# Performance work log

Measured on AMD Instinct MI355X. Metric: run time of the kernel, lower is better.

The kernel has to match this reference:

```python
import jax, jax.numpy as jnp
import numpy as np

LATENT, D_MODEL, WIN, ENC_IN, BATCH = 128, 512, 256, 55, 256


def setup_inputs() -> dict:
    key = jax.random.key(0)
    ks = jax.random.split(key, 9)
    sl = lambda k, shape, fan_in: (jax.random.normal(k, shape, jnp.float32) / np.sqrt(fan_in)).astype(jnp.float32)
    return {
        "z": jax.random.normal(ks[0], (BATCH, LATENT), jnp.float32),
        "h_proj_w": sl(ks[1], (D_MODEL, LATENT), LATENT),
        "h_proj_b": sl(ks[2], (D_MODEL,), LATENT),
        "w_ih": sl(ks[3], (3 * D_MODEL, D_MODEL), D_MODEL),
        "w_hh": sl(ks[4], (3 * D_MODEL, D_MODEL), D_MODEL),
        "b_ih": sl(ks[5], (3 * D_MODEL,), D_MODEL),
        "b_hh": sl(ks[6], (3 * D_MODEL,), D_MODEL),
        "out_w": sl(ks[7], (ENC_IN, D_MODEL), D_MODEL),
        "out_b": sl(ks[8], (ENC_IN,), D_MODEL),
        "win_size": WIN,
    }


def reference(z, h_proj_w, h_proj_b, w_ih, w_hh, b_ih, b_hh, out_w, out_b, win_size):
    d = h_proj_w.shape[0]
    # h0 = tanh(Linear(z)) -> [B, d]
    h0 = jnp.tanh(z @ h_proj_w.T + h_proj_b)
    # GRU input is all zeros, so input-gate preactivation is just b_ih
    # (w_ih @ 0 == 0); gate order in torch GRU is (r, z, n).
    gi_r, gi_z, gi_n = b_ih[:d], b_ih[d:2 * d], b_ih[2 * d:]

    def step(h, _):
        gh = h @ w_hh.T + b_hh                      # [B, 3d]
        r = jax.nn.sigmoid(gi_r + gh[:, :d])
        zg = jax.nn.sigmoid(gi_z + gh[:, d:2 * d])
        n = jnp.tanh(gi_n + r * gh[:, 2 * d:])
        h_new = (1.0 - zg) * n + zg * h
        return h_new, h_new

    _, hs = jax.lax.scan(step, h0, None, length=win_size)  # [T, B, d]
    hs = jnp.transpose(hs, (1, 0, 2))                      # [B, T, d]
    return hs @ out_w.T + out_b                            # [B, T, enc_in]
```

## Files before the change

### kernel.cpp

```cpp
#include <hip/hip_runtime.h>

#define DM     512
#define LAT    128
#define WIN_   256
#define ENC    55
#define GB     32
#define BT     8
#define DS     64
#define TPB    768
#define OUT_T  256
#define AROW16 528
#define GHS    200
#define OWS    520
#define NK     22
#define NKP    24

typedef __attribute__((ext_vector_type(8))) short bf8;
typedef __attribute__((ext_vector_type(4))) float f4;
typedef unsigned long long u64;
typedef unsigned short u16;

__device__ __align__(128) u64 g_ring2[2][GB][8][BT][NKP];
__device__ __align__(128) u64 g_lcnt[GB * 8 * 16];

__device__ __forceinline__ u16 f2bf(float f) {
    union { float f; unsigned int i; } v; v.f = f;
    unsigned int r = v.i + 0x7fffu + ((v.i >> 16) & 1u);
    return (u16)(r >> 16);
}
__device__ __forceinline__ float sigm(float x) { return 1.f / (1.f + __expf(-x)); }
__device__ __forceinline__ float tanh_(float x) {
    x = fminf(x, 40.f);
    float e = __expf(2.f * x);
    return (e - 1.f) / (e + 1.f);
}
#define ALOAD(p)     __hip_atomic_load((p),      __ATOMIC_RELAXED, __HIP_MEMORY_SCOPE_AGENT)
#define ASTORE(p, v) __hip_atomic_store((p), (v), __ATOMIC_RELAXED, __HIP_MEMORY_SCOPE_AGENT)

__global__ __launch_bounds__(TPB, 3) void gru_fused(
    const float* __restrict__ z,
    const float* __restrict__ hpw,
    const float* __restrict__ hpb,
    const float* __restrict__ whh,
    const float* __restrict__ bih,
    const float* __restrict__ bhh,
    const float* __restrict__ outw,
    const float* __restrict__ outb,
    float* __restrict__ out)
{
    const int blk  = blockIdx.x;
    const int g    = blk & (GB - 1);
    const int s    = blk >> 5;
    const int d0   = s * DS;
    const int row0 = g * BT;
    const int tid  = threadIdx.x;
    const int wave = tid >> 6;
    const int lane = tid & 63;
    const int quad = lane >> 4;
    const int nl   = lane & 15;

    __shared__ __align__(16) u16 sm16[BT * AROW16];
    __shared__ __align__(16) float ghT[BT][GHS];
    __shared__ float bias_r[DS], bias_z[DS], gin_[DS], bhn_[DS];
    __shared__ __align__(16) u16 hpack[BT][66];
    __shared__ __align__(16) u16 sOutW[ENC * OWS];
    __shared__ float sOutB[64];
    __shared__ u64 sh_lc;

    u64* lc_own = g_lcnt + (u64)(g * 8 + s) * 16;
    if (tid == 0) sh_lc = ALOAD(lc_own);

    if (tid < DS) {
        int dg = d0 + tid;
        bias_r[tid] = bih[dg]       + bhh[dg];
        bias_z[tid] = bih[512 + dg] + bhh[512 + dg];
        gin_[tid]   = bih[1024 + dg];
        bhn_[tid]   = bhh[1024 + dg];
    }
    if (tid < ENC) sOutB[tid] = outb[tid];
    for (int i = tid; i < ENC * DM; i += TPB)
        sOutW[(i >> 9) * OWS + (i & 511)] = f2bf(outw[i]);

    const int gl   = wave * 16 + nl;
    const int sel  = gl >> 6;
    const int jrow = sel * 512 + d0 + (gl & 63);
    bf8 bfrag[16];
#pragma unroll
    for (int kb = 0; kb < 16; ++kb) {
        const float* wp = whh + jrow * DM + kb * 32 + quad * 8;
        bf8 v;
#pragma unroll
        for (int j = 0; j < 8; ++j) v[j] = (short)f2bf(wp[j]);
        bfrag[kb] = v;
    }
    __syncthreads();

    const u64 base = sh_lc * 512ULL + 1ULL;
    float hprev_reg = 0.f;

    if (wave < BT) {
        float acc = hpb[d0 + lane];
        const float* zr = z + (row0 + wave) * LAT;
        const float* wr = hpw + (d0 + lane) * LAT;
#pragma unroll 8
        for (int k = 0; k < LAT; ++k) acc += zr[k] * wr[k];
        hprev_reg = tanh_(acc);
        if (lane < 2) hpack[wave][64 + lane] = 0;
        hpack[wave][lane] = f2bf(hprev_reg);
        const u16 sq = (u16)base;
        if (lane < NK) {
            u16 b0 = hpack[wave][3 * lane], b1 = hpack[wave][3 * lane + 1],
                b2 = hpack[wave][3 * lane + 2];
            u64 rec = (u64)sq | ((u64)b0 << 16) | ((u64)b1 << 32) | ((u64)b2 << 48);
            ASTORE(&g_ring2[0][g][s][wave][lane], rec);
        }
    }

    const u16* afrag_base = sm16 + (nl & 7) * AROW16;

    for (int t = 1; t <= WIN_; ++t) {
        const int sp = (t - 1) & 1, sc = t & 1;
        const u16 want = (u16)(base + t - 1);

        if (wave < BT)
            sm16[wave * AROW16 + d0 + lane] = f2bf(hprev_reg);
        if (wave >= 1 && wave < 8) {
            const int j = (s + wave) & 7;
            const u64* rb = &g_ring2[sp][g][j][0][0];
            const int row = lane >> 3, k = lane & 7;
            {
                const u64* pp = rb + 7 * NKP + 21;
                long guard = 0;
                while ((u16)ALOAD(pp) != want && guard < (1L << 18)) ++guard;
            }
            const u64* p0 = rb + row * NKP + k;
            const bool v2 = (k + 16) < NK;
            u64 r0 = ALOAD(p0), r1 = ALOAD(p0 + 8), r2 = v2 ? ALOAD(p0 + 16) : 0;
            bool ok0 = ((u16)r0 == want), ok1 = ((u16)r1 == want),
                 ok2 = (!v2) || ((u16)r2 == want);
            long guard = 0;
            while (!__all(ok0 && ok1 && ok2) && guard < (1L << 18)) {
                if (!ok0) { r0 = ALOAD(p0);      ok0 = ((u16)r0 == want); }
                if (!ok1) { r1 = ALOAD(p0 + 8);  ok1 = ((u16)r1 == want); }
                if (!ok2) { r2 = ALOAD(p0 + 16); ok2 = ((u16)r2 == want); }
                ++guard;
            }
            u16* dst = sm16 + row * AROW16 + j * 64;
            int db = 3 * k;
            dst[db] = (u16)(r0 >> 16); dst[db + 1] = (u16)(r0 >> 32); dst[db + 2] = (u16)(r0 >> 48);
            db = 3 * (k + 8);
            dst[db] = (u16)(r1 >> 16); dst[db + 1] = (u16)(r1 >> 32); dst[db + 2] = (u16)(r1 >> 48);
            if (v2) {
                db = 3 * (k + 16);
                dst[db] = (u16)(r2 >> 16);
                if (db + 1 < DS) dst[db + 1] = (u16)(r2 >> 32);
                if (db + 2 < DS) dst[db + 2] = (u16)(r2 >> 48);
            }
        }
        __syncthreads();

        f4 acc = {0.f, 0.f, 0.f, 0.f};
#pragma unroll
        for (int kb = 0; kb < 16; ++kb) {
            bf8 av = *(const bf8*)(afrag_base + quad * 8 + kb * 32);
            acc = __builtin_amdgcn_mfma_f32_16x16x32_bf16(av, bfrag[kb], acc, 0, 0, 0);
        }
        if (quad < 2) {
#pragma unroll
            for (int r = 0; r < 4; ++r) ghT[quad * 4 + r][gl] = acc[r];
        }
        __syncthreads();

        if (wave < BT) {
            const int d = lane;
            const float* grow = &ghT[wave][0];
            float rr = sigm(bias_r[d] + grow[d]);
            float zg = sigm(bias_z[d] + grow[64 + d]);
            float nn = tanh_(gin_[d] + rr * (bhn_[d] + grow[128 + d]));
            float h  = (1.f - zg) * nn + zg * hprev_reg;
            hprev_reg = h;
            hpack[wave][d] = f2bf(h);
            const u16 sq = (u16)(base + t);
            if (lane < NK) {
                u16 b0 = hpack[wave][3 * lane], b1 = hpack[wave][3 * lane + 1],
                    b2 = hpack[wave][3 * lane + 2];
                u64 rec = (u64)sq | ((u64)b0 << 16) | ((u64)b1 << 32) | ((u64)b2 << 48);
                ASTORE(&g_ring2[sc][g][s][wave][lane], rec);
            }
        }

        const int tau = t - 2;
        const bool proj = (tau >= 0) && ((tau & 7) == s);
        if (proj && wave >= 8) {
            const int e  = (wave - 8) * 16 + nl;
            const int ec = (e < ENC) ? e : (ENC - 1);
            const u16* wrow = sOutW + ec * OWS + quad * 8;
            f4 accp = {0.f, 0.f, 0.f, 0.f};
#pragma unroll
            for (int kb = 0; kb < 16; ++kb) {
                bf8 av = *(const bf8*)(afrag_base + quad * 8 + kb * 32);
                bf8 wv = *(const bf8*)(wrow + kb * 32);
                accp = __builtin_amdgcn_mfma_f32_16x16x32_bf16(av, wv, accp, 0, 0, 0);
            }
            if (quad < 2 && e < ENC) {
                float ob = sOutB[e];
#pragma unroll
                for (int r = 0; r < 4; ++r) {
                    int m = quad * 4 + r;
                    out[(row0 + m) * (OUT_T * ENC) + tau * ENC + e] = accp[r] + ob;
                }
            }
        }
        if (proj) __syncthreads();
    }

    if (s == 7) {
        const u16 want = (u16)(base + WIN_);
        if (wave < BT)
            sm16[wave * AROW16 + d0 + lane] = f2bf(hprev_reg);
        if (wave >= 1 && wave < 8) {
            const int j = (s + wave) & 7;
            const u64* rb = &g_ring2[0][g][j][0][0];
            const int row = lane >> 3, k = lane & 7;
            {
                const u64* pp = rb + 7 * NKP + 21;
                long guard = 0;
                while ((u16)ALOAD(pp) != want && guard < (1L << 18)) ++guard;
            }
            const u64* p0 = rb + row * NKP + k;
            const bool v2 = (k + 16) < NK;
            u64 r0 = ALOAD(p0), r1 = ALOAD(p0 + 8), r2 = v2 ? ALOAD(p0 + 16) : 0;
            bool ok0 = ((u16)r0 == want), ok1 = ((u16)r1 == want),
                 ok2 = (!v2) || ((u16)r2 == want);
            long guard = 0;
            while (!__all(ok0 && ok1 && ok2) && guard < (1L << 18)) {
                if (!ok0) { r0 = ALOAD(p0);      ok0 = ((u16)r0 == want); }
                if (!ok1) { r1 = ALOAD(p0 + 8);  ok1 = ((u16)r1 == want); }
                if (!ok2) { r2 = ALOAD(p0 + 16); ok2 = ((u16)r2 == want); }
                ++guard;
            }
            u16* dst = sm16 + row * AROW16 + j * 64;
            int db = 3 * k;
            dst[db] = (u16)(r0 >> 16); dst[db + 1] = (u16)(r0 >> 32); dst[db + 2] = (u16)(r0 >> 48);
            db = 3 * (k + 8);
            dst[db] = (u16)(r1 >> 16); dst[db + 1] = (u16)(r1 >> 32); dst[db + 2] = (u16)(r1 >> 48);
            if (v2) {
                db = 3 * (k + 16);
                dst[db] = (u16)(r2 >> 16);
                if (db + 1 < DS) dst[db + 1] = (u16)(r2 >> 32);
                if (db + 2 < DS) dst[db + 2] = (u16)(r2 >> 48);
            }
        }
        __syncthreads();
        if (wave >= 8) {
            const int e  = (wave - 8) * 16 + nl;
            const int ec = (e < ENC) ? e : (ENC - 1);
            const u16* wrow = sOutW + ec * OWS + quad * 8;
            f4 accp = {0.f, 0.f, 0.f, 0.f};
#pragma unroll
            for (int kb = 0; kb < 16; ++kb) {
                bf8 av = *(const bf8*)(afrag_base + quad * 8 + kb * 32);
                bf8 wv = *(const bf8*)(wrow + kb * 32);
                accp = __builtin_amdgcn_mfma_f32_16x16x32_bf16(av, wv, accp, 0, 0, 0);
            }
            if (quad < 2 && e < ENC) {
                float ob = sOutB[e];
#pragma unroll
                for (int r = 0; r < 4; ++r) {
                    int m = quad * 4 + r;
                    out[(row0 + m) * (OUT_T * ENC) + 255 * ENC + e] = accp[r] + ob;
                }
            }
        }
    }

    if (tid == 0) ASTORE(lc_own, sh_lc + 1ULL);
}

extern "C" void kernel_launch(void* const* d_in, const int* in_sizes, int n_in,
                              void* d_out, int out_size, void* d_ws, size_t ws_size,
                              hipStream_t stream) {
    const float* z    = (const float*)d_in[0];
    const float* hpw  = (const float*)d_in[1];
    const float* hpb  = (const float*)d_in[2];
    const float* whh  = (const float*)d_in[4];
    const float* bih  = (const float*)d_in[5];
    const float* bhh  = (const float*)d_in[6];
    const float* outw = (const float*)d_in[7];
    const float* outb = (const float*)d_in[8];
    float* out = (float*)d_out;

    (void)d_ws; (void)ws_size;
    gru_fused<<<dim3(256), dim3(TPB), 0, stream>>>(
        z, hpw, hpb, whh, bih, bhh, outw, outb, out);
}
```

Measured before the change: 705.0 us.

## Streamline per-step sync: lighter barriers, shuffle packing, speculative ring loads

Replaces __syncthreads with a barrier that waits only on LDS counters, so outstanding global stores do not stall the workgroup barrier. Packs the bf16 hidden-state records with wave shuffles instead of an LDS staging buffer. Polls the ring by loading the sentinel and the payload together, cutting a round trip of global latency per step. Splits the MFMA chain into two accumulators to expose more instruction-level parallelism. It adds an explicit vmcnt wait before publishing and relies on memory-ordering assumptions that could be fragile.

```diff
diff --git a/kernel.cpp b/kernel.cpp
--- a/kernel.cpp
+++ b/kernel.cpp
@@ -36,6 +36,50 @@
 }
 #define ALOAD(p)     __hip_atomic_load((p),      __ATOMIC_RELAXED, __HIP_MEMORY_SCOPE_AGENT)
 #define ASTORE(p, v) __hip_atomic_store((p), (v), __ATOMIC_RELAXED, __HIP_MEMORY_SCOPE_AGENT)
+
+__device__ __forceinline__ void bar_lgkm() {
+    __builtin_amdgcn_sched_barrier(0);
+    asm volatile("s_waitcnt lgkmcnt(0)" ::: "memory");
+    __builtin_amdgcn_s_barrier();
+    __builtin_amdgcn_sched_barrier(0);
+}
+
+__device__ __forceinline__ void fetch_slice(const u64* rb, u16 want, u16* sm,
+                                            int j, int lane) {
+    const int row = lane >> 3, k = lane & 7;
+    const u64* pp = rb + 7 * NKP + 21;
+    const u64* p0 = rb + row * NKP + k;
+    const bool v2 = (k + 16) < NK;
+    u64 r0 = 0, r1 = 0, r2 = 0;
+    long guard = 0;
+    for (;;) {
+        u64 bc = ALOAD(pp);
+        r0 = ALOAD(p0);
+        r1 = ALOAD(p0 + 8);
+        r2 = v2 ? ALOAD(p0 + 16) : 0;
+        if ((u16)bc == want || ++guard >= (1L << 18)) break;
+    }
+    bool ok0 = ((u16)r0 == want), ok1 = ((u16)r1 == want),
+         ok2 = (!v2) || ((u16)r2 == want);
+    guard = 0;
+    while (!__all(ok0 && ok1 && ok2) && guard < (1L << 18)) {
+        if (!ok0) { r0 = ALOAD(p0);      ok0 = ((u16)r0 == want); }
+        if (!ok1) { r1 = ALOAD(p0 + 8);  ok1 = ((u16)r1 == want); }
+        if (!ok2) { r2 = ALOAD(p0 + 16); ok2 = ((u16)r2 == want); }
+        ++guard;
+    }
+    u16* dst = sm + row * AROW16 + j * 64;
+    int db = 3 * k;
+    dst[db] = (u16)(r0 >> 16); dst[db + 1] = (u16)(r0 >> 32); dst[db + 2] = (u16)(r0 >> 48);
+    db = 3 * (k + 8);
+    dst[db] = (u16)(r1 >> 16); dst[db + 1] = (u16)(r1 >> 32); dst[db + 2] = (u16)(r1 >> 48);
+    if (v2) {
+        db = 3 * (k + 16);
+        dst[db] = (u16)(r2 >> 16);
+        if (db + 1 < DS) dst[db + 1] = (u16)(r2 >> 32);
+        if (db + 2 < DS) dst[db + 2] = (u16)(r2 >> 48);
+    }
+}
 
 __global__ __launch_bounds__(TPB, 3) void gru_fused(
     const float* __restrict__ z,
@@ -62,7 +106,6 @@
     __shared__ __align__(16) u16 sm16[BT * AROW16];
     __shared__ __align__(16) float ghT[BT][GHS];
     __shared__ float bias_r[DS], bias_z[DS], gin_[DS], bhn_[DS];
-    __shared__ __align__(16) u16 hpack[BT][66];
     __shared__ __align__(16) u16 sOutW[ENC * OWS];
     __shared__ float sOutB[64];
     __shared__ u64 sh_lc;
@@ -93,7 +136,7 @@
         for (int j = 0; j < 8; ++j) v[j] = (short)f2bf(wp[j]);
         bfrag[kb] = v;
     }
-    __syncthreads();
+    bar_lgkm();
 
     const u64 base = sh_lc * 512ULL + 1ULL;
     float hprev_reg = 0.f;
@@ -105,13 +148,13 @@
 #pragma unroll 8
         for (int k = 0; k < LAT; ++k) acc += zr[k] * wr[k];
         hprev_reg = tanh_(acc);
-        if (lane < 2) hpack[wave][64 + lane] = 0;
-        hpack[wave][lane] = f2bf(hprev_reg);
-        const u16 sq = (u16)base;
+        int hbf = (int)f2bf(hprev_reg);
+        int b0 = __shfl(hbf, 3 * lane);
+        int b1 = __shfl(hbf, 3 * lane + 1);
+        int b2 = __shfl(hbf, 3 * lane + 2);
         if (lane < NK) {
-            u16 b0 = hpack[wave][3 * lane], b1 = hpack[wave][3 * lane + 1],
-                b2 = hpack[wave][3 * lane + 2];
-            u64 rec = (u64)sq | ((u64)b0 << 16) | ((u64)b1 << 32) | ((u64)b2 << 48);
+            u64 rec = (u64)(u16)base | ((u64)(u16)b0 << 16)
+                    | ((u64)(u16)b1 << 32) | ((u64)(u16)b2 << 48);
             ASTORE(&g_ring2[0][g][s][wave][lane], rec);
         }
     }
@@ -126,50 +169,24 @@
             sm16[wave * AROW16 + d0 + lane] = f2bf(hprev_reg);
         if (wave >= 1 && wave < 8) {
             const int j = (s + wave) & 7;
-            const u64* rb = &g_ring2[sp][g][j][0][0];
-            const int row = lane >> 3, k = lane & 7;
-            {
-                const u64* pp = rb + 7 * NKP + 21;
-                long guard = 0;
-                while ((u16)ALOAD(pp) != want && guard < (1L << 18)) ++guard;
-            }
-            const u64* p0 = rb + row * NKP + k;
-            const bool v2 = (k + 16) < NK;
-            u64 r0 = ALOAD(p0), r1 = ALOAD(p0 + 8), r2 = v2 ? ALOAD(p0 + 16) : 0;
-            bool ok0 = ((u16)r0 == want), ok1 = ((u16)r1 == want),
-                 ok2 = (!v2) || ((u16)r2 == want);
-            long guard = 0;
-            while (!__all(ok0 && ok1 && ok2) && guard < (1L << 18)) {
-                if (!ok0) { r0 = ALOAD(p0);      ok0 = ((u16)r0 == want); }
-                if (!ok1) { r1 = ALOAD(p0 + 8);  ok1 = ((u16)r1 == want); }
-                if (!ok2) { r2 = ALOAD(p0 + 16); ok2 = ((u16)r2 == want); }
-                ++guard;
-            }
-            u16* dst = sm16 + row * AROW16 + j * 64;
-            int db = 3 * k;
-            dst[db] = (u16)(r0 >> 16); dst[db + 1] = (u16)(r0 >> 32); dst[db + 2] = (u16)(r0 >> 48);
-            db = 3 * (k + 8);
-            dst[db] = (u16)(r1 >> 16); dst[db + 1] = (u16)(r1 >> 32); dst[db + 2] = (u16)(r1 >> 48);
-            if (v2) {
-                db = 3 * (k + 16);
-                dst[db] = (u16)(r2 >> 16);
-                if (db + 1 < DS) dst[db + 1] = (u16)(r2 >> 32);
-                if (db + 2 < DS) dst[db + 2] = (u16)(r2 >> 48);
-            }
-        }
-        __syncthreads();
-
-        f4 acc = {0.f, 0.f, 0.f, 0.f};
-#pragma unroll
-        for (int kb = 0; kb < 16; ++kb) {
-            bf8 av = *(const bf8*)(afrag_base + quad * 8 + kb * 32);
-            acc = __builtin_amdgcn_mfma_f32_16x16x32_bf16(av, bfrag[kb], acc, 0, 0, 0);
+            fetch_slice(&g_ring2[sp][g][j][0][0], want, sm16, j, lane);
+        }
+        bar_lgkm();
+
+        f4 acc0 = {0.f, 0.f, 0.f, 0.f}, acc1 = {0.f, 0.f, 0.f, 0.f};
+#pragma unroll
+        for (int kb = 0; kb < 16; kb += 2) {
+            bf8 av0 = *(const bf8*)(afrag_base + quad * 8 + kb * 32);
+            bf8 av1 = *(const bf8*)(afrag_base + quad * 8 + (kb + 1) * 32);
+            acc0 = __builtin_amdgcn_mfma_f32_16x16x32_bf16(av0, bfrag[kb],     acc0, 0, 0, 0);
+            acc1 = __builtin_amdgcn_mfma_f32_16x16x32_bf16(av1, bfrag[kb + 1], acc1, 0, 0, 0);
         }
         if (quad < 2) {
+            f4 acc = acc0 + acc1;
 #pragma unroll
             for (int r = 0; r < 4; ++r) ghT[quad * 4 + r][gl] = acc[r];
         }
-        __syncthreads();
+        bar_lgkm();
 
         if (wave < BT) {
             const int d = lane;
@@ -179,12 +196,14 @@
             float nn = tanh_(gin_[d] + rr * (bhn_[d] + grow[128 + d]));
             float h  = (1.f - zg) * nn + zg * hprev_reg;
             hprev_reg = h;
-            hpack[wave][d] = f2bf(h);
-            const u16 sq = (u16)(base + t);
+            int hbf = (int)f2bf(h);
+            int b0 = __shfl(hbf, 3 * lane);
+            int b1 = __shfl(hbf, 3 * lane + 1);
+            int b2 = __shfl(hbf, 3 * lane + 2);
             if (lane < NK) {
-                u16 b0 = hpack[wave][3 * lane], b1 = hpack[wave][3 * lane + 1],
-                    b2 = hpack[wave][3 * lane + 2];
-                u64 rec = (u64)sq | ((u64)b0 << 16) | ((u64)b1 << 32) | ((u64)b2 << 48);
+                u64 rec = (u64)(u16)(base + t) | ((u64)(u16)b0 << 16)
+                        | ((u64)(u16)b1 << 32) | ((u64)(u16)b2 << 48);
+                asm volatile("s_waitcnt vmcnt(0)" ::: "memory");
                 ASTORE(&g_ring2[sc][g][s][wave][lane], rec);
             }
         }
@@ -211,7 +230,7 @@
                 }
             }
         }
-        if (proj) __syncthreads();
+        if (proj) bar_lgkm();
     }
 
     if (s == 7) {
@@ -220,38 +239,9 @@
             sm16[wave * AROW16 + d0 + lane] = f2bf(hprev_reg);
         if (wave >= 1 && wave < 8) {
             const int j = (s + wave) & 7;
-            const u64* rb = &g_ring2[0][g][j][0][0];
-            const int row = lane >> 3, k = lane & 7;
-            {
-                const u64* pp = rb + 7 * NKP + 21;
-                long guard = 0;
-                while ((u16)ALOAD(pp) != want && guard < (1L << 18)) ++guard;
-            }
-            const u64* p0 = rb + row * NKP + k;
-            const bool v2 = (k + 16) < NK;
-            u64 r0 = ALOAD(p0), r1 = ALOAD(p0 + 8), r2 = v2 ? ALOAD(p0 + 16) : 0;
-            bool ok0 = ((u16)r0 == want), ok1 = ((u16)r1 == want),
-                 ok2 = (!v2) || ((u16)r2 == want);
-            long guard = 0;
-            while (!__all(ok0 && ok1 && ok2) && guard < (1L << 18)) {
-                if (!ok0) { r0 = ALOAD(p0);      ok0 = ((u16)r0 == want); }
-                if (!ok1) { r1 = ALOAD(p0 + 8);  ok1 = ((u16)r1 == want); }
-                if (!ok2) { r2 = ALOAD(p0 + 16); ok2 = ((u16)r2 == want); }
-                ++guard;
-            }
-            u16* dst = sm16 + row * AROW16 + j * 64;
-            int db = 3 * k;
-            dst[db] = (u16)(r0 >> 16); dst[db + 1] = (u16)(r0 >> 32); dst[db + 2] = (u16)(r0 >> 48);
-            db = 3 * (k + 8);
-            dst[db] = (u16)(r1 >> 16); dst[db + 1] = (u16)(r1 >> 32); dst[db + 2] = (u16)(r1 >> 48);
-            if (v2) {
-                db = 3 * (k + 16);
-                dst[db] = (u16)(r2 >> 16);
-                if (db + 1 < DS) dst[db + 1] = (u16)(r2 >> 32);
-                if (db + 2 < DS) dst[db + 2] = (u16)(r2 >> 48);
-            }
-        }
-        __syncthreads();
+            fetch_slice(&g_ring2[0][g][j][0][0], want, sm16, j, lane);
+        }
+        bar_lgkm();
         if (wave >= 8) {
             const int e  = (wave - 8) * 16 + nl;
             const int ec = (e < ENC) ? e : (ENC - 1);
```

After: 866.6 us. +22.9%, slower.
